# Kernel tuning notes

Hardware: AMD Instinct MI355X
Metric: run time of the kernel (lower is better)

## Reference

```python
import jax, jax.numpy as jnp
import numpy as np

# ---- Cl(3,0) Cayley table derivation (pure Python, done once at import) ----
_BASIS_GENS = [(), (1,), (2,), (3,), (1, 2), (1, 3), (2, 3), (1, 2, 3)]
_GENS_TO_IDX = {g: i for i, g in enumerate(_BASIS_GENS)}

def _reduce_product(a_gens, b_gens):
    gens = list(a_gens) + list(b_gens)
    sign = 1
    changed = True
    while changed:
        changed = False
        i = 0
        while i < len(gens) - 1:
            if gens[i] == gens[i + 1]:
                gens.pop(i); gens.pop(i)
                changed = True
                if i > 0:
                    i -= 1
            elif gens[i] > gens[i + 1]:
                gens[i], gens[i + 1] = gens[i + 1], gens[i]
                sign *= -1
                changed = True
                i += 1
            else:
                i += 1
    return _GENS_TO_IDX[tuple(gens)], sign

def _k_groups():
    gi = [[] for _ in range(8)]
    gj = [[] for _ in range(8)]
    gs = [[] for _ in range(8)]
    for i in range(8):
        for j in range(8):
            k, s = _reduce_product(_BASIS_GENS[i], _BASIS_GENS[j])
            gi[k].append(i); gj[k].append(j); gs[k].append(float(s))
    return np.array(gi), np.array(gj), np.array(gs, dtype=np.float32)

KG_I, KG_J, KG_S = _k_groups()  # each (8, 8): for target blade k, 8 (i,j,sign) contributions
LN_EPS = 1e-5


def setup_inputs() -> dict:
    key = jax.random.key(0)
    ks = jax.random.split(key, 6)
    B, T, N, D, Fdim = 4, 4096, 8, 128, 512
    return {
        "x": jax.random.normal(ks[0], (B, T, N, D), dtype=jnp.float32),
        "interaction_weights": 0.1 * jax.random.normal(ks[1], (N, N), dtype=jnp.float32),
        "w_gate": 0.02 * jax.random.normal(ks[2], (D, Fdim), dtype=jnp.float32),
        "w_up": 0.02 * jax.random.normal(ks[3], (D, Fdim), dtype=jnp.float32),
        "w_down": 0.02 * jax.random.normal(ks[4], (Fdim, D), dtype=jnp.float32),
        "ln_gamma": jnp.ones((D,), dtype=jnp.float32),
        "ln_beta": jnp.zeros((D,), dtype=jnp.float32),
        "geo_gate": jnp.float32(0.5),
    }


def reference(x, interaction_weights, w_gate, w_up, w_down, ln_gamma, ln_beta, geo_gate):
    # x: (B, T, 8, D)
    kg_i = jnp.asarray(KG_I)
    kg_j = jnp.asarray(KG_J)
    kg_s = jnp.asarray(KG_S)

    # K-grouped Cayley geometric self-product
    w = jax.nn.sigmoid(interaction_weights)          # (8, 8)
    sw = kg_s * w[kg_i, kg_j]                        # (8, 8): sign * weight per (k, pair)
    x_i = x[:, :, kg_i, :]                           # (B, T, 8, 8, D)
    x_j = x[:, :, kg_j, :]                           # (B, T, 8, 8, D)
    geo = jnp.sum(x_i * x_j * sw[None, None, :, :, None], axis=3)  # (B, T, 8, D)

    # gate-mix geo with residual stream
    gate = jax.nn.sigmoid(geo_gate)
    mixed = gate * geo + (1.0 - gate) * x

    # LayerNorm over last dim
    mu = jnp.mean(mixed, axis=-1, keepdims=True)
    var = jnp.var(mixed, axis=-1, keepdims=True)
    normed = (mixed - mu) / jnp.sqrt(var + LN_EPS) * ln_gamma + ln_beta

    # per-blade SwiGLU FFN
    g = normed @ w_gate                              # (B, T, 8, F)
    u = normed @ w_up
    out = (jax.nn.silu(g) * u) @ w_down              # (B, T, 8, D)
    return x + out
```

## Files before the change

kernel.cpp:

```cpp
#include <hip/hip_runtime.h>


typedef __bf16 bf16x8 __attribute__((ext_vector_type(8)));
typedef float  f32x4  __attribute__((ext_vector_type(4)));

#define MFMA16(a, b, c) __builtin_amdgcn_mfma_f32_16x16x32_bf16((a), (b), (c), 0, 0, 0)

constexpr int OFF_WG = 0;
constexpr int OFF_WU = 131072;
constexpr int OFF_WD = 262144;
constexpr int OFF_C  = 393216;


__device__ __forceinline__ float fexp2(float x) {
  float r; asm("v_exp_f32 %0, %1" : "=v"(r) : "v"(x)); return r;
}
__device__ __forceinline__ float frcp(float x) {
  float r; asm("v_rcp_f32 %0, %1" : "=v"(r) : "v"(x)); return r;
}
__device__ __forceinline__ float fsigmoid(float x) {
  return frcp(1.f + fexp2(-1.44269504088896f * x));
}
__device__ __forceinline__ unsigned cvtbf(float f) {
  unsigned u = __builtin_bit_cast(unsigned, f);
  return (u + 0x7fffu + ((u >> 16) & 1u)) >> 16;
}
__device__ __forceinline__ unsigned pack2(float a, float b) {
  return cvtbf(a) | (cvtbf(b) << 16);
}

__device__ constexpr int PIdx[7][4][2] = {
  {{0,1},{2,4},{3,5},{6,7}},
  {{0,2},{1,4},{3,6},{5,7}},
  {{0,3},{1,5},{2,6},{4,7}},
  {{0,4},{1,2},{3,7},{5,6}},
  {{0,5},{1,3},{2,7},{4,6}},
  {{0,6},{1,7},{2,3},{4,5}},
  {{0,7},{1,6},{2,5},{3,4}}};

__global__ __launch_bounds__(256) void k_prep(
    const float* __restrict__ W,
    const float* __restrict__ wg,
    const float* __restrict__ wu,
    const float* __restrict__ wd,
    const float* __restrict__ gg,
    char* __restrict__ ws) {
  int gid = blockIdx.x * 256 + threadIdx.x;
  if (gid < 65536) {
    int f = gid & 511, k = gid >> 9;
    unsigned short v = (unsigned short)cvtbf(wg[k * 512 + f]);
    int fl = f & 63;
    int off = OFF_WG + (f >> 6) * 16384 + (((fl * 256 + k * 2)) ^ ((f & 7) << 4));
    *(unsigned short*)(ws + off) = v;
  } else if (gid < 131072) {
    int t = gid - 65536;
    int f = t & 511, k = t >> 9;
    unsigned short v = (unsigned short)cvtbf(wu[k * 512 + f]);
    int fl = f & 63;
    int off = OFF_WU + (f >> 6) * 16384 + (((fl * 256 + k * 2)) ^ ((f & 7) << 4));
    *(unsigned short*)(ws + off) = v;
  } else {
    int t = gid - 131072;
    int d = t & 127, f = t >> 7;
    unsigned short v = (unsigned short)cvtbf(wd[f * 128 + d]);
    int fl = f & 63;
    int off = OFF_WD + (f >> 6) * 16384 + (((d * 128 + fl * 2)) ^ ((d & 7) << 4));
    *(unsigned short*)(ws + off) = v;
  }
  if (blockIdx.x == 0 && threadIdx.x == 0) {
    float s[64];
    for (int i = 0; i < 64; ++i) s[i] = fsigmoid(W[i]);
    float* C = (float*)(ws + OFF_C);
#define Sij(i, j) s[(i) * 8 + (j)]
    for (int i = 0; i < 8; ++i) C[i] = (i < 4 ? 1.f : -1.f) * Sij(i, i);
    C[8]  =  Sij(0,1) + Sij(1,0);  C[9]  = -Sij(2,4) + Sij(4,2);
    C[10] = -Sij(3,5) + Sij(5,3);  C[11] = -Sij(6,7) - Sij(7,6);
    C[12] =  Sij(0,2) + Sij(2,0);  C[13] =  Sij(1,4) - Sij(4,1);
    C[14] = -Sij(3,6) + Sij(6,3);  C[15] =  Sij(5,7) + Sij(7,5);
    C[16] =  Sij(0,3) + Sij(3,0);  C[17] =  Sij(1,5) - Sij(5,1);
    C[18] =  Sij(2,6) - Sij(6,2);  C[19] = -Sij(4,7) - Sij(7,4);
    C[20] =  Sij(0,4) + Sij(4,0);  C[21] =  Sij(1,2) - Sij(2,1);
    C[22] =  Sij(3,7) + Sij(7,3);  C[23] = -Sij(5,6) + Sij(6,5);
    C[24] =  Sij(0,5) + Sij(5,0);  C[25] =  Sij(1,3) - Sij(3,1);
    C[26] = -Sij(2,7) - Sij(7,2);  C[27] =  Sij(4,6) - Sij(6,4);
    C[28] =  Sij(0,6) + Sij(6,0);  C[29] =  Sij(1,7) + Sij(7,1);
    C[30] =  Sij(2,3) - Sij(3,2);  C[31] = -Sij(4,5) + Sij(5,4);
    C[32] =  Sij(0,7) + Sij(7,0);  C[33] =  Sij(1,6) + Sij(6,1);
    C[34] = -Sij(2,5) - Sij(5,2);  C[35] =  Sij(3,4) + Sij(4,3);
#undef Sij
    float gate = fsigmoid(gg[0]);
    C[36] = gate; C[37] = 1.f - gate;
  }
}

__global__ __launch_bounds__(256) void k_geo_ln(
    const float* __restrict__ x,
    const float* __restrict__ gamma,
    const float* __restrict__ beta,
    const float* __restrict__ cws,
    unsigned* __restrict__ outw) {
  const int tid = threadIdx.x, l = tid & 63, w = tid >> 6;
  const long bt = (long)blockIdx.x * 4 + w;
  const long row0 = bt * 8;

  float C[38];
#pragma unroll
  for (int i = 0; i < 38; ++i) C[i] = cws[i];
  const float gate = C[36], omg = C[37];

  float2 gm = *(const float2*)(gamma + 2 * l);
  float2 be = *(const float2*)(beta + 2 * l);

  float xa[8], xb[8];
#pragma unroll
  for (int n = 0; n < 8; ++n) {
    float2 v = *(const float2*)(x + (size_t)(row0 + n) * 128 + 2 * l);
    xa[n] = v.x; xb[n] = v.y;
  }

  float ga[8], gb[8];
  {
    float a0 = C[0] * xa[0] * xa[0], b0 = C[0] * xb[0] * xb[0];
#pragma unroll
    for (int i = 1; i < 8; ++i) {
      a0 = fmaf(C[i], xa[i] * xa[i], a0);
      b0 = fmaf(C[i], xb[i] * xb[i], b0);
    }
    ga[0] = a0; gb[0] = b0;
#pragma unroll
    for (int k = 1; k < 8; ++k) {
      float ta = 0.f, tb = 0.f;
#pragma unroll
      for (int p = 0; p < 4; ++p) {
        const int i = PIdx[k - 1][p][0], j = PIdx[k - 1][p][1];
        const float c = C[8 + (k - 1) * 4 + p];
        ta = fmaf(c, xa[i] * xa[j], ta);
        tb = fmaf(c, xb[i] * xb[j], tb);
      }
      ga[k] = ta; gb[k] = tb;
    }
  }

  float ma[8], mb[8], s[8], ss[8];
#pragma unroll
  for (int n = 0; n < 8; ++n) {
    ma[n] = fmaf(gate, ga[n], omg * xa[n]);
    mb[n] = fmaf(gate, gb[n], omg * xb[n]);
    s[n]  = ma[n] + mb[n];
    ss[n] = fmaf(ma[n], ma[n], mb[n] * mb[n]);
  }
#pragma unroll
  for (int st = 0; st < 6; ++st) {
    const int off = 1 << st;
#pragma unroll
    for (int n = 0; n < 8; ++n) {
      s[n]  += __shfl_xor(s[n], off);
      ss[n] += __shfl_xor(ss[n], off);
    }
  }
#pragma unroll
  for (int n = 0; n < 8; ++n) {
    float mean = s[n] * (1.f / 128.f);
    float var  = fmaf(-mean, mean, ss[n] * (1.f / 128.f));
    float rstd = rsqrtf(var + 1e-5f);
    float na = fmaf((ma[n] - mean) * rstd, gm.x, be.x);
    float nb = fmaf((mb[n] - mean) * rstd, gm.y, be.y);
    outw[(size_t)(row0 + n) * 128 + l] = pack2(na, nb);
  }
}

__global__ __launch_bounds__(256, 2) void k_mlp(
    const float* __restrict__ x,
    float* __restrict__ out,
    const char* __restrict__ ws) {
  __shared__ __align__(16) char lds[65536];
  const int tid = threadIdx.x, l = tid & 63, w = tid >> 6;
  const int r16 = l & 15, g4 = l >> 4;
  const long rows_base = (long)blockIdx.x * 128;
  const long wrow0 = rows_base + w * 32;

  const char* outb = (const char*)out;
  bf16x8 bn[2][4];
#pragma unroll
  for (int rt = 0; rt < 2; ++rt)
#pragma unroll
    for (int ks = 0; ks < 4; ++ks) {
      const uint4 v = *(const uint4*)(outb + (wrow0 + rt * 16 + r16) * 512 +
                                      (ks * 32 + g4 * 8) * 2);
      bn[rt][ks] = __builtin_bit_cast(bf16x8, v);
    }

  f32x4 acc[8][2];
#pragma unroll
  for (int dt = 0; dt < 8; ++dt)
#pragma unroll
    for (int rt = 0; rt < 2; ++rt) acc[dt][rt] = f32x4{0.f, 0.f, 0.f, 0.f};

  const char* lwg = lds;
  const char* lwu = lds + 16384;
  const char* lwd = lds + 32768;
  char* lht = lds + 49152 + w * 4096;

  for (int fc = 0; fc < 8; ++fc) {
    __syncthreads();
#pragma unroll
    for (int j = 0; j < 12; ++j) {
      int o = (w * 12 + j) * 1024 + l * 16;
      const char* src = ws + (o >> 14) * 131072 + fc * 16384 + (o & 16383);
      __builtin_amdgcn_global_load_lds(
          (const __attribute__((address_space(1))) unsigned*)src,
          (__attribute__((address_space(3))) unsigned*)(lds + (w * 12 + j) * 1024),
          16, 0, 0);
    }
    __syncthreads();

#pragma unroll
    for (int ft = 0; ft < 4; ++ft) {
      const int fl = ft * 16 + r16, swzf = (fl & 7) << 4;
      bf16x8 ag[4], au[4];
#pragma unroll
      for (int ks = 0; ks < 4; ++ks) {
        const int kb = (ks * 32 + g4 * 8) * 2;
        ag[ks] = *(const bf16x8*)(lwg + fl * 256 + (kb ^ swzf));
        au[ks] = *(const bf16x8*)(lwu + fl * 256 + (kb ^ swzf));
      }
#pragma unroll
      for (int rt = 0; rt < 2; ++rt) {
        f32x4 cg = {0.f, 0.f, 0.f, 0.f}, cu = {0.f, 0.f, 0.f, 0.f};
#pragma unroll
        for (int ks = 0; ks < 4; ++ks) {
          cg = MFMA16(ag[ks], bn[rt][ks], cg);
          cu = MFMA16(au[ks], bn[rt][ks], cu);
        }
        float h0 = cg[0] * cu[0] * frcp(1.f + fexp2(-1.44269504f * cg[0]));
        float h1 = cg[1] * cu[1] * frcp(1.f + fexp2(-1.44269504f * cg[1]));
        float h2 = cg[2] * cu[2] * frcp(1.f + fexp2(-1.44269504f * cg[2]));
        float h3 = cg[3] * cu[3] * frcp(1.f + fexp2(-1.44269504f * cg[3]));
        uint2 hv; hv.x = pack2(h0, h1); hv.y = pack2(h2, h3);
        const int row_l = rt * 16 + r16;
        const int fb = (ft * 16 + g4 * 4) * 2;
        *(uint2*)(lht + row_l * 128 + (fb ^ ((row_l & 7) << 4))) = hv;
      }
    }

    bf16x8 hb[2][2];
#pragma unroll
    for (int rt = 0; rt < 2; ++rt)
#pragma unroll
      for (int ks2 = 0; ks2 < 2; ++ks2) {
        const int row_l = rt * 16 + r16;
        const int fb = (ks2 * 32 + g4 * 8) * 2;
        hb[rt][ks2] = *(const bf16x8*)(lht + row_l * 128 + (fb ^ ((row_l & 7) << 4)));
      }
#pragma unroll
    for (int dt = 0; dt < 8; ++dt) {
      const int d = dt * 16 + r16, swzd = (d & 7) << 4;
      bf16x8 w0 = *(const bf16x8*)(lwd + d * 128 + (((g4 * 8) * 2) ^ swzd));
      bf16x8 w1 = *(const bf16x8*)(lwd + d * 128 + (((32 + g4 * 8) * 2) ^ swzd));
      acc[dt][0] = MFMA16(w0, hb[0][0], acc[dt][0]);
      acc[dt][0] = MFMA16(w1, hb[0][1], acc[dt][0]);
      acc[dt][1] = MFMA16(w0, hb[1][0], acc[dt][1]);
      acc[dt][1] = MFMA16(w1, hb[1][1], acc[dt][1]);
    }
  }

#pragma unroll
  for (int dt = 0; dt < 8; ++dt)
#pragma unroll
    for (int rt = 0; rt < 2; ++rt) {
      const size_t row = (size_t)(wrow0 + rt * 16 + r16);
      const int db = dt * 16 + g4 * 4;
      const float4 xv = *(const float4*)(x + row * 128 + db);
      float4 o;
      o.x = acc[dt][rt][0] + xv.x;
      o.y = acc[dt][rt][1] + xv.y;
      o.z = acc[dt][rt][2] + xv.z;
      o.w = acc[dt][rt][3] + xv.w;
      *(float4*)(out + row * 128 + db) = o;
    }
}


extern "C" void kernel_launch(void* const* d_in, const int* in_sizes, int n_in,
                              void* d_out, int out_size, void* d_ws, size_t ws_size,
                              hipStream_t stream) {
  (void)in_sizes; (void)n_in; (void)out_size; (void)ws_size;
  const float* x     = (const float*)d_in[0];
  const float* W     = (const float*)d_in[1];
  const float* wg    = (const float*)d_in[2];
  const float* wu    = (const float*)d_in[3];
  const float* wd    = (const float*)d_in[4];
  const float* gamma = (const float*)d_in[5];
  const float* beta  = (const float*)d_in[6];
  const float* gg    = (const float*)d_in[7];
  char* ws = (char*)d_ws;

  k_prep<<<768, 256, 0, stream>>>(W, wg, wu, wd, gg, ws);
  k_geo_ln<<<4096, 256, 0, stream>>>(x, gamma, beta, (const float*)(ws + OFF_C),
                                     (unsigned*)d_out);
  k_mlp<<<1024, 256, 0, stream>>>(x, (float*)d_out, ws);
}
```

Baseline: 200.0 us.

## Fuse geometric product and LayerNorm into MLP kernel with larger per-wave row tiles

Merges the geo-product/LayerNorm kernel into the MLP kernel so normalized bf16 activations are built directly in registers. This removes the intermediate write and re-read through the output buffer, and one launch. Each wave now handles 64 rows instead of 32, so each staged weight chunk is reused across twice as many rows. The first weight chunk is prefetched while the LN prologue runs. LDS grows to 80KB and accumulator registers double, which may hurt occupancy with only 512 blocks.

```diff
diff --git a/kernel.cpp b/kernel.cpp
--- a/kernel.cpp
+++ b/kernel.cpp
@@ -10,7 +10,6 @@
 constexpr int OFF_WU = 131072;
 constexpr int OFF_WD = 262144;
 constexpr int OFF_C  = 393216;
-
 
 __device__ __forceinline__ float fexp2(float x) {
   float r; asm("v_exp_f32 %0, %1" : "=v"(r) : "v"(x)); return r;
@@ -39,32 +38,29 @@
   {{0,7},{1,6},{2,5},{3,4}}};
 
 __global__ __launch_bounds__(256) void k_prep(
-    const float* __restrict__ W,
-    const float* __restrict__ wg,
-    const float* __restrict__ wu,
-    const float* __restrict__ wd,
-    const float* __restrict__ gg,
-    char* __restrict__ ws) {
+    const float* __restrict__ W, const float* __restrict__ wg,
+    const float* __restrict__ wu, const float* __restrict__ wd,
+    const float* __restrict__ gg, char* __restrict__ ws) {
   int gid = blockIdx.x * 256 + threadIdx.x;
   if (gid < 65536) {
     int f = gid & 511, k = gid >> 9;
     unsigned short v = (unsigned short)cvtbf(wg[k * 512 + f]);
     int fl = f & 63;
-    int off = OFF_WG + (f >> 6) * 16384 + (((fl * 256 + k * 2)) ^ ((f & 7) << 4));
+    int off = OFF_WG + (f >> 6) * 16384 + ((fl * 256 + k * 2) ^ ((f & 7) << 4));
     *(unsigned short*)(ws + off) = v;
   } else if (gid < 131072) {
     int t = gid - 65536;
     int f = t & 511, k = t >> 9;
     unsigned short v = (unsigned short)cvtbf(wu[k * 512 + f]);
     int fl = f & 63;
-    int off = OFF_WU + (f >> 6) * 16384 + (((fl * 256 + k * 2)) ^ ((f & 7) << 4));
+    int off = OFF_WU + (f >> 6) * 16384 + ((fl * 256 + k * 2) ^ ((f & 7) << 4));
     *(unsigned short*)(ws + off) = v;
   } else {
     int t = gid - 131072;
     int d = t & 127, f = t >> 7;
     unsigned short v = (unsigned short)cvtbf(wd[f * 128 + d]);
     int fl = f & 63;
-    int off = OFF_WD + (f >> 6) * 16384 + (((d * 128 + fl * 2)) ^ ((d & 7) << 4));
+    int off = OFF_WD + (f >> 6) * 16384 + ((d * 128 + fl * 2) ^ ((d & 7) << 4));
     *(unsigned short*)(ws + off) = v;
   }
   if (blockIdx.x == 0 && threadIdx.x == 0) {
@@ -93,181 +89,193 @@
   }
 }
 
-__global__ __launch_bounds__(256) void k_geo_ln(
+__global__ __launch_bounds__(256, 2) void k_fused(
     const float* __restrict__ x,
     const float* __restrict__ gamma,
     const float* __restrict__ beta,
     const float* __restrict__ cws,
-    unsigned* __restrict__ outw) {
+    float* __restrict__ out,
+    const char* __restrict__ ws) {
+  __shared__ __align__(16) char lds[81920];
   const int tid = threadIdx.x, l = tid & 63, w = tid >> 6;
-  const long bt = (long)blockIdx.x * 4 + w;
-  const long row0 = bt * 8;
+  const int r16 = l & 15, g4 = l >> 4;
+  const long wrow0 = (long)blockIdx.x * 256 + (long)w * 64;
+
+  char* scr = lds + 49152 + w * 8192;
+
+#define STAGE(fcv)                                                             \
+  _Pragma("unroll") for (int j = 0; j < 12; ++j) {                             \
+    int o = (w * 12 + j) * 1024 + l * 16;                                      \
+    const char* src = ws + (o >> 14) * 131072 + (fcv) * 16384 + (o & 16383);   \
+    __builtin_amdgcn_global_load_lds(                                          \
+        (const __attribute__((address_space(1))) unsigned*)src,                \
+        (__attribute__((address_space(3))) unsigned*)(lds + (w * 12 + j) * 1024), \
+        16, 0, 0);                                                             \
+  }
+
+  STAGE(0);
 
   float C[38];
 #pragma unroll
   for (int i = 0; i < 38; ++i) C[i] = cws[i];
   const float gate = C[36], omg = C[37];
 
-  float2 gm = *(const float2*)(gamma + 2 * l);
-  float2 be = *(const float2*)(beta + 2 * l);
-
-  float xa[8], xb[8];
-#pragma unroll
-  for (int n = 0; n < 8; ++n) {
-    float2 v = *(const float2*)(x + (size_t)(row0 + n) * 128 + 2 * l);
-    xa[n] = v.x; xb[n] = v.y;
-  }
-
-  float ga[8], gb[8];
-  {
-    float a0 = C[0] * xa[0] * xa[0], b0 = C[0] * xb[0] * xb[0];
-#pragma unroll
-    for (int i = 1; i < 8; ++i) {
-      a0 = fmaf(C[i], xa[i] * xa[i], a0);
-      b0 = fmaf(C[i], xb[i] * xb[i], b0);
-    }
-    ga[0] = a0; gb[0] = b0;
-#pragma unroll
-    for (int k = 1; k < 8; ++k) {
-      float ta = 0.f, tb = 0.f;
-#pragma unroll
-      for (int p = 0; p < 4; ++p) {
-        const int i = PIdx[k - 1][p][0], j = PIdx[k - 1][p][1];
-        const float c = C[8 + (k - 1) * 4 + p];
-        ta = fmaf(c, xa[i] * xa[j], ta);
-        tb = fmaf(c, xb[i] * xb[j], tb);
-      }
-      ga[k] = ta; gb[k] = tb;
-    }
-  }
-
-  float ma[8], mb[8], s[8], ss[8];
-#pragma unroll
-  for (int n = 0; n < 8; ++n) {
-    ma[n] = fmaf(gate, ga[n], omg * xa[n]);
-    mb[n] = fmaf(gate, gb[n], omg * xb[n]);
-    s[n]  = ma[n] + mb[n];
-    ss[n] = fmaf(ma[n], ma[n], mb[n] * mb[n]);
-  }
-#pragma unroll
-  for (int st = 0; st < 6; ++st) {
-    const int off = 1 << st;
-#pragma unroll
-    for (int n = 0; n < 8; ++n) {
-      s[n]  += __shfl_xor(s[n], off);
-      ss[n] += __shfl_xor(ss[n], off);
-    }
-  }
-#pragma unroll
-  for (int n = 0; n < 8; ++n) {
-    float mean = s[n] * (1.f / 128.f);
-    float var  = fmaf(-mean, mean, ss[n] * (1.f / 128.f));
-    float rstd = rsqrtf(var + 1e-5f);
-    float na = fmaf((ma[n] - mean) * rstd, gm.x, be.x);
-    float nb = fmaf((mb[n] - mean) * rstd, gm.y, be.y);
-    outw[(size_t)(row0 + n) * 128 + l] = pack2(na, nb);
-  }
-}
-
-__global__ __launch_bounds__(256, 2) void k_mlp(
-    const float* __restrict__ x,
-    float* __restrict__ out,
-    const char* __restrict__ ws) {
-  __shared__ __align__(16) char lds[65536];
-  const int tid = threadIdx.x, l = tid & 63, w = tid >> 6;
-  const int r16 = l & 15, g4 = l >> 4;
-  const long rows_base = (long)blockIdx.x * 128;
-  const long wrow0 = rows_base + w * 32;
-
-  const char* outb = (const char*)out;
-  bf16x8 bn[2][4];
-#pragma unroll
-  for (int rt = 0; rt < 2; ++rt)
+  bf16x8 bn[4][4];
+#pragma unroll
+  for (int p = 0; p < 4; ++p) {
+#pragma unroll
+    for (int hB = 0; hB < 2; ++hB) {
+      const long r0 = wrow0 + p * 16 + hB * 8;
+      float xa[8], xb[8];
+#pragma unroll
+      for (int n = 0; n < 8; ++n) {
+        float2 v = *(const float2*)(x + (size_t)(r0 + n) * 128 + 2 * l);
+        xa[n] = v.x; xb[n] = v.y;
+      }
+      float ga[8], gb[8];
+      {
+        float a0 = C[0] * xa[0] * xa[0], b0 = C[0] * xb[0] * xb[0];
+#pragma unroll
+        for (int i = 1; i < 8; ++i) {
+          a0 = fmaf(C[i], xa[i] * xa[i], a0);
+          b0 = fmaf(C[i], xb[i] * xb[i], b0);
+        }
+        ga[0] = a0; gb[0] = b0;
+#pragma unroll
+        for (int k = 1; k < 8; ++k) {
+          float ta = 0.f, tb = 0.f;
+#pragma unroll
+          for (int q = 0; q < 4; ++q) {
+            const int i = PIdx[k - 1][q][0], jj = PIdx[k - 1][q][1];
+            const float c = C[8 + (k - 1) * 4 + q];
+            ta = fmaf(c, xa[i] * xa[jj], ta);
+            tb = fmaf(c, xb[i] * xb[jj], tb);
+          }
+          ga[k] = ta; gb[k] = tb;
+        }
+      }
+#pragma unroll
+      for (int n = 0; n < 8; ++n) {
+        float2 m2;
+        m2.x = fmaf(gate, ga[n], omg * xa[n]);
+        m2.y = fmaf(gate, gb[n], omg * xb[n]);
+        const int sr = hB * 8 + n;
+        *(float2*)(scr + sr * 512 + ((l * 8) ^ (n << 4))) = m2;
+      }
+    }
+    f32x4 mx[4][2];
+    float s = 0.f, ss = 0.f;
+    const int swr = (r16 & 7) << 4;
+#pragma unroll
+    for (int ks = 0; ks < 4; ++ks)
+#pragma unroll
+      for (int hh = 0; hh < 2; ++hh) {
+        f32x4 v = *(const f32x4*)(scr + r16 * 512 +
+                                  ((ks * 128 + g4 * 32 + hh * 16) ^ swr));
+        mx[ks][hh] = v;
+#pragma unroll
+        for (int e = 0; e < 4; ++e) { s += v[e]; ss = fmaf(v[e], v[e], ss); }
+      }
+    s  += __shfl_xor(s, 16);  s  += __shfl_xor(s, 32);
+    ss += __shfl_xor(ss, 16); ss += __shfl_xor(ss, 32);
+    const float mean = s * (1.f / 128.f);
+    const float var  = fmaf(-mean, mean, ss * (1.f / 128.f));
+    const float rstd = rsqrtf(var + 1e-5f);
 #pragma unroll
     for (int ks = 0; ks < 4; ++ks) {
-      const uint4 v = *(const uint4*)(outb + (wrow0 + rt * 16 + r16) * 512 +
-                                      (ks * 32 + g4 * 8) * 2);
-      bn[rt][ks] = __builtin_bit_cast(bf16x8, v);
-    }
-
-  f32x4 acc[8][2];
+      const float4 gm0 = *(const float4*)(gamma + ks * 32 + g4 * 8);
+      const float4 gm1 = *(const float4*)(gamma + ks * 32 + g4 * 8 + 4);
+      const float4 be0 = *(const float4*)(beta + ks * 32 + g4 * 8);
+      const float4 be1 = *(const float4*)(beta + ks * 32 + g4 * 8 + 4);
+      float nv[8];
+      nv[0] = fmaf((mx[ks][0][0] - mean) * rstd, gm0.x, be0.x);
+      nv[1] = fmaf((mx[ks][0][1] - mean) * rstd, gm0.y, be0.y);
+      nv[2] = fmaf((mx[ks][0][2] - mean) * rstd, gm0.z, be0.z);
+      nv[3] = fmaf((mx[ks][0][3] - mean) * rstd, gm0.w, be0.w);
+      nv[4] = fmaf((mx[ks][1][0] - mean) * rstd, gm1.x, be1.x);
+      nv[5] = fmaf((mx[ks][1][1] - mean) * rstd, gm1.y, be1.y);
+      nv[6] = fmaf((mx[ks][1][2] - mean) * rstd, gm1.z, be1.z);
+      nv[7] = fmaf((mx[ks][1][3] - mean) * rstd, gm1.w, be1.w);
+      uint4 uv;
+      uv.x = pack2(nv[0], nv[1]); uv.y = pack2(nv[2], nv[3]);
+      uv.z = pack2(nv[4], nv[5]); uv.w = pack2(nv[6], nv[7]);
+      bn[p][ks] = __builtin_bit_cast(bf16x8, uv);
+    }
+  }
+
+  __syncthreads();
+
+  f32x4 acc[8][4];
 #pragma unroll
   for (int dt = 0; dt < 8; ++dt)
 #pragma unroll
-    for (int rt = 0; rt < 2; ++rt) acc[dt][rt] = f32x4{0.f, 0.f, 0.f, 0.f};
+    for (int rt = 0; rt < 4; ++rt) acc[dt][rt] = f32x4{0.f, 0.f, 0.f, 0.f};
 
   const char* lwg = lds;
   const char* lwu = lds + 16384;
   const char* lwd = lds + 32768;
-  char* lht = lds + 49152 + w * 4096;
+  char* lht = scr;
 
   for (int fc = 0; fc < 8; ++fc) {
-    __syncthreads();
-#pragma unroll
-    for (int j = 0; j < 12; ++j) {
-      int o = (w * 12 + j) * 1024 + l * 16;
-      const char* src = ws + (o >> 14) * 131072 + fc * 16384 + (o & 16383);
-      __builtin_amdgcn_global_load_lds(
-          (const __attribute__((address_space(1))) unsigned*)src,
-          (__attribute__((address_space(3))) unsigned*)(lds + (w * 12 + j) * 1024),
-          16, 0, 0);
-    }
-    __syncthreads();
-
 #pragma unroll
     for (int ft = 0; ft < 4; ++ft) {
       const int fl = ft * 16 + r16, swzf = (fl & 7) << 4;
       bf16x8 ag[4], au[4];
 #pragma unroll
       for (int ks = 0; ks < 4; ++ks) {
-        const int kb = (ks * 32 + g4 * 8) * 2;
+        const int kb = ks * 64 + g4 * 16;
         ag[ks] = *(const bf16x8*)(lwg + fl * 256 + (kb ^ swzf));
         au[ks] = *(const bf16x8*)(lwu + fl * 256 + (kb ^ swzf));
       }
 #pragma unroll
-      for (int rt = 0; rt < 2; ++rt) {
+      for (int rt = 0; rt < 4; ++rt) {
         f32x4 cg = {0.f, 0.f, 0.f, 0.f}, cu = {0.f, 0.f, 0.f, 0.f};
 #pragma unroll
         for (int ks = 0; ks < 4; ++ks) {
           cg = MFMA16(ag[ks], bn[rt][ks], cg);
           cu = MFMA16(au[ks], bn[rt][ks], cu);
         }
-        float h0 = cg[0] * cu[0] * frcp(1.f + fexp2(-1.44269504f * cg[0]));
-        float h1 = cg[1] * cu[1] * frcp(1.f + fexp2(-1.44269504f * cg[1]));
-        float h2 = cg[2] * cu[2] * frcp(1.f + fexp2(-1.44269504f * cg[2]));
-        float h3 = cg[3] * cu[3] * frcp(1.f + fexp2(-1.44269504f * cg[3]));
+        const float h0 = cg[0] * cu[0] * frcp(1.f + fexp2(-1.44269504f * cg[0]));
+        const float h1 = cg[1] * cu[1] * frcp(1.f + fexp2(-1.44269504f * cg[1]));
+        const float h2 = cg[2] * cu[2] * frcp(1.f + fexp2(-1.44269504f * cg[2]));
+        const float h3 = cg[3] * cu[3] * frcp(1.f + fexp2(-1.44269504f * cg[3]));
         uint2 hv; hv.x = pack2(h0, h1); hv.y = pack2(h2, h3);
-        const int row_l = rt * 16 + r16;
-        const int fb = (ft * 16 + g4 * 4) * 2;
-        *(uint2*)(lht + row_l * 128 + (fb ^ ((row_l & 7) << 4))) = hv;
-      }
-    }
-
-    bf16x8 hb[2][2];
-#pragma unroll
-    for (int rt = 0; rt < 2; ++rt)
-#pragma unroll
-      for (int ks2 = 0; ks2 < 2; ++ks2) {
-        const int row_l = rt * 16 + r16;
-        const int fb = (ks2 * 32 + g4 * 8) * 2;
-        hb[rt][ks2] = *(const bf16x8*)(lht + row_l * 128 + (fb ^ ((row_l & 7) << 4)));
+        const int row = rt * 16 + r16;
+        *(uint2*)(lht + row * 128 + ((ft * 32 + g4 * 8) ^ ((row & 7) << 4))) = hv;
+      }
+    }
+    bf16x8 hb[4][2];
+#pragma unroll
+    for (int rt = 0; rt < 4; ++rt)
+#pragma unroll
+      for (int k2 = 0; k2 < 2; ++k2) {
+        const int row = rt * 16 + r16;
+        hb[rt][k2] = *(const bf16x8*)(lht + row * 128 +
+                                      ((k2 * 64 + g4 * 16) ^ ((row & 7) << 4)));
       }
 #pragma unroll
     for (int dt = 0; dt < 8; ++dt) {
       const int d = dt * 16 + r16, swzd = (d & 7) << 4;
-      bf16x8 w0 = *(const bf16x8*)(lwd + d * 128 + (((g4 * 8) * 2) ^ swzd));
-      bf16x8 w1 = *(const bf16x8*)(lwd + d * 128 + (((32 + g4 * 8) * 2) ^ swzd));
-      acc[dt][0] = MFMA16(w0, hb[0][0], acc[dt][0]);
-      acc[dt][0] = MFMA16(w1, hb[0][1], acc[dt][0]);
-      acc[dt][1] = MFMA16(w0, hb[1][0], acc[dt][1]);
-      acc[dt][1] = MFMA16(w1, hb[1][1], acc[dt][1]);
-    }
-  }
+      bf16x8 w0 = *(const bf16x8*)(lwd + d * 128 + ((g4 * 16) ^ swzd));
+      bf16x8 w1 = *(const bf16x8*)(lwd + d * 128 + ((64 + g4 * 16) ^ swzd));
+#pragma unroll
+      for (int rt = 0; rt < 4; ++rt) {
+        acc[dt][rt] = MFMA16(w0, hb[rt][0], acc[dt][rt]);
+        acc[dt][rt] = MFMA16(w1, hb[rt][1], acc[dt][rt]);
+      }
+    }
+    if (fc < 7) {
+      __syncthreads();
+      STAGE(fc + 1);
+      __syncthreads();
+    }
+  }
+#undef STAGE
 
 #pragma unroll
   for (int dt = 0; dt < 8; ++dt)
 #pragma unroll
-    for (int rt = 0; rt < 2; ++rt) {
+    for (int rt = 0; rt < 4; ++rt) {
       const size_t row = (size_t)(wrow0 + rt * 16 + r16);
       const int db = dt * 16 + g4 * 4;
       const float4 xv = *(const float4*)(x + row * 128 + db);
@@ -296,7 +304,6 @@
   char* ws = (char*)d_ws;
 
   k_prep<<<768, 256, 0, stream>>>(W, wg, wu, wd, gg, ws);
-  k_geo_ln<<<4096, 256, 0, stream>>>(x, gamma, beta, (const float*)(ws + OFF_C),
-                                     (unsigned*)d_out);
-  k_mlp<<<1024, 256, 0, stream>>>(x, (float*)d_out, ws);
-}
+  k_fused<<<512, 256, 0, stream>>>(x, gamma, beta, (const float*)(ws + OFF_C),
+                                   (float*)d_out, ws);
+}
```

Result: slower. 205.5 us (+2.8%).
